# Kernel tuning notes

Hardware: AMD Instinct MI355X
Metric: run time of the kernel (lower is better)

Reference implementation:

```python
import jax, jax.numpy as jnp
import numpy as np

N_USERS = 100000
N_ITEMS = 40000
N_NODES = N_USERS + N_ITEMS
D = 64
IMG_DIM = 2048
TXT_DIM = 384
N_EDGES = 1000000
N_LAYERS = 2
ALPHA = 0.2


def setup_inputs() -> dict:
    key = jax.random.key(0)
    ks = jax.random.split(key, 10)
    edge_index = jax.random.randint(ks[0], (2, N_EDGES), 0, N_NODES, dtype=jnp.int64 if jax.config.jax_enable_x64 else jnp.int32)
    edge_weight = jax.random.uniform(ks[1], (N_EDGES, 1), dtype=jnp.float32)
    image_feats = jax.random.normal(ks[2], (N_ITEMS, IMG_DIM), dtype=jnp.float32)
    text_feats = jax.random.normal(ks[3], (N_ITEMS, TXT_DIM), dtype=jnp.float32)
    s_img = 1.0 / np.sqrt(IMG_DIM)
    s_txt = 1.0 / np.sqrt(TXT_DIM)
    image_trs_w = jax.random.uniform(ks[4], (IMG_DIM, D), jnp.float32, -s_img, s_img)
    image_trs_b = jnp.zeros((D,), jnp.float32)
    text_trs_w = jax.random.uniform(ks[5], (TXT_DIM, D), jnp.float32, -s_txt, s_txt)
    text_trs_b = jnp.zeros((D,), jnp.float32)
    image_pref = jax.random.normal(ks[6], (N_USERS, D), jnp.float32) * 0.1
    text_pref = jax.random.normal(ks[7], (N_USERS, D), jnp.float32) * 0.1
    return {
        "edge_index": edge_index,
        "edge_weight": edge_weight,
        "image_feats": image_feats,
        "text_feats": text_feats,
        "image_trs_w": image_trs_w,
        "image_trs_b": image_trs_b,
        "text_trs_w": text_trs_w,
        "text_trs_b": text_trs_b,
        "image_pref": image_pref,
        "text_pref": text_pref,
    }


def _l2_normalize(x):
    # matches F.normalize(x, p=2, dim=1, eps=1e-12)
    n = jnp.linalg.norm(x, axis=1, keepdims=True)
    return x / jnp.maximum(n, 1e-12)


def _propagate(x, src, dst, w):
    # PyG 'add' aggregation: message = x[src] * w, scatter-add into dst
    msgs = x[src] * w  # [E, D]
    return jax.ops.segment_sum(msgs, dst, num_segments=N_NODES)


def reference(edge_index, edge_weight, image_feats, text_feats,
              image_trs_w, image_trs_b, text_trs_w, text_trs_b,
              image_pref, text_pref):
    src, dst = edge_index[0], edge_index[1]

    image_emb = _l2_normalize(image_feats @ image_trs_w + image_trs_b)
    text_emb = _l2_normalize(text_feats @ text_trs_w + text_trs_b)

    ego_img = jnp.concatenate([image_pref, image_emb], axis=0)  # [N, D]
    ego_txt = jnp.concatenate([text_pref, text_emb], axis=0)    # [N, D]

    for _ in range(N_LAYERS):
        ego_img = _propagate(ego_img, src, dst, edge_weight) + ALPHA * ego_img
        ego_txt = _propagate(ego_txt, src, dst, edge_weight) + ALPHA * ego_txt

    # stack final modality embeddings; rows 0:N_USERS are user preferences,
    # N_USERS: are item embeddings (torch.split boundary)
    return jnp.stack([ego_img, ego_txt], axis=0)  # [2, N, D]
```

## Files before the change

kernel.cpp:

```cpp
#include <hip/hip_runtime.h>

#define N_USERS 100000
#define N_ITEMS 40000
#define NN      140000
#define N_EDGES 1000000
#define ALPHA   0.2f

typedef short bf16x8 __attribute__((ext_vector_type(8)));
typedef float f32x4  __attribute__((ext_vector_type(4)));

__device__ __forceinline__ unsigned short f2b(float x) {
    unsigned u = __builtin_bit_cast(unsigned, x);
    unsigned r = (u + 0x7FFFu + ((u >> 16) & 1u)) >> 16;
    return (unsigned short)r;
}
__device__ __forceinline__ unsigned cvtpk(float lo, float hi) {
    unsigned r;
    asm("v_cvt_pk_bf16_f32 %0, %1, %2" : "=v"(r) : "v"(lo), "v"(hi));
    return r;
}
__device__ __forceinline__ float blo(unsigned u) { return __builtin_bit_cast(float, u << 16); }
__device__ __forceinline__ float bhi(unsigned u) { return __builtin_bit_cast(float, u & 0xFFFF0000u); }

#define PREP_CP   6250
#define PREP_CI   (PREP_CP + 512)
#define PREP_CT   (PREP_CI + 96)
#define PREP_ALL  (PREP_CT + 3907)

__global__ __launch_bounds__(256)
void prep(const float* __restrict__ imgp, const float* __restrict__ txtp,
          unsigned short* __restrict__ X,
          const float* __restrict__ Wi, short* __restrict__ WtImg,
          const float* __restrict__ Wx, short* __restrict__ WtTxt,
          const int* __restrict__ ei, int* __restrict__ deg)
{
    int b = blockIdx.x, t = threadIdx.x;
    if (b < PREP_CP) {
        int tid = b * 256 + t;
        if (tid >= N_USERS * 16) return;
        int i  = tid >> 4;
        int c8 = tid & 15;
        const float* src = (c8 < 8) ? &imgp[(size_t)i * 64 + c8 * 8]
                                    : &txtp[(size_t)i * 64 + (c8 - 8) * 8];
        float4 a = *reinterpret_cast<const float4*>(src);
        float4 c = *reinterpret_cast<const float4*>(src + 4);
        int4 o = make_int4((int)cvtpk(a.x, a.y), (int)cvtpk(a.z, a.w),
                           (int)cvtpk(c.x, c.y), (int)cvtpk(c.z, c.w));
        *reinterpret_cast<int4*>(&X[(size_t)i * 128 + c8 * 8]) = o;
    } else if (b < PREP_CI) {
        int tid = (b - PREP_CP) * 256 + t;
        int k = tid >> 6, n = tid & 63;
        WtImg[(k >> 5) * 2048 + n * 32 + ((k >> 3) & 3) * 8 + (k & 7)] = (short)f2b(Wi[tid]);
    } else if (b < PREP_CT) {
        int tid = (b - PREP_CI) * 256 + t;
        if (tid >= 384 * 64) return;
        int k = tid >> 6, n = tid & 63;
        WtTxt[(k >> 5) * 2048 + n * 32 + ((k >> 3) & 3) * 8 + (k & 7)] = (short)f2b(Wx[tid]);
    } else {
        int e = (b - PREP_CT) * 256 + t;
        if (e < N_EDGES) atomicAdd(&deg[ei[N_EDGES + e]], 1);
    }
}

template<int K, int COLOFF>
__device__ __forceinline__
void gemm_body(int bx, const float* __restrict__ A, const short* __restrict__ Wt,
               const float* __restrict__ bias, unsigned short* __restrict__ X)
{
    constexpr int STEPS = K / 32;
    const int t    = threadIdx.x;
    const int wid  = t >> 6;
    const int lane = t & 63;
    const int lo   = lane & 15;
    const int g    = lane >> 4;
    const int r0w  = bx * 64 + wid * 16;

    const float* Ap  = A + (size_t)(r0w + lo) * K + g * 8;
    const short* Bp0 = Wt + lo * 32 + g * 8;

    f32x4 acc[4];
    #pragma unroll
    for (int ct = 0; ct < 4; ++ct) acc[ct] = (f32x4){0.f, 0.f, 0.f, 0.f};

    float4 xA, yA, xB, yB;
    bf16x8 bA[4], bB[4];

    auto loadA = [&](int s, float4& x, float4& y) {
        const float* p = Ap + s * 32;
        x = *reinterpret_cast<const float4*>(p);
        y = *reinterpret_cast<const float4*>(p + 4);
    };
    auto loadB = [&](int s, bf16x8* bb) {
        const short* p = Bp0 + s * 2048;
        #pragma unroll
        for (int ct = 0; ct < 4; ++ct) {
            int4 w = *reinterpret_cast<const int4*>(p + ct * 512);
            bb[ct] = __builtin_bit_cast(bf16x8, w);
        }
    };
    auto domfma = [&](const float4& x, const float4& y, const bf16x8* bb) {
        int4 ai = make_int4((int)cvtpk(x.x, x.y), (int)cvtpk(x.z, x.w),
                            (int)cvtpk(y.x, y.y), (int)cvtpk(y.z, y.w));
        bf16x8 a = __builtin_bit_cast(bf16x8, ai);
        #pragma unroll
        for (int ct = 0; ct < 4; ++ct)
            acc[ct] = __builtin_amdgcn_mfma_f32_16x16x32_bf16(a, bb[ct], acc[ct], 0, 0, 0);
    };

    loadA(0, xA, yA);
    loadB(0, bA);
    for (int s = 0; s < STEPS; s += 2) {
        loadA(s + 1, xB, yB);
        loadB(s + 1, bB);
        domfma(xA, yA, bA);
        if (s + 2 < STEPS) {
            loadA(s + 2, xA, yA);
            loadB(s + 2, bA);
        }
        domfma(xB, yB, bB);
    }

    float bia[4];
    #pragma unroll
    for (int ct = 0; ct < 4; ++ct) bia[ct] = bias[ct * 16 + lo];

    #pragma unroll
    for (int r = 0; r < 4; ++r) {
        float v[4];
        float ss = 0.f;
        #pragma unroll
        for (int ct = 0; ct < 4; ++ct) { v[ct] = acc[ct][r] + bia[ct]; ss += v[ct] * v[ct]; }
        ss += __shfl_xor(ss, 1);
        ss += __shfl_xor(ss, 2);
        ss += __shfl_xor(ss, 4);
        ss += __shfl_xor(ss, 8);
        float sc = 1.0f / fmaxf(sqrtf(ss), 1e-12f);
        int grow = r0w + g * 4 + r;
        unsigned short* dst = &X[(size_t)(N_USERS + grow) * 128 + COLOFF + lo];
        #pragma unroll
        for (int ct = 0; ct < 4; ++ct) dst[ct * 16] = f2b(v[ct] * sc);
    }
}

__global__ __launch_bounds__(256, 2)
void gemm_fill(const float* __restrict__ Ai, const short* __restrict__ WtImg,
               const float* __restrict__ bi,
               const float* __restrict__ Ax, const short* __restrict__ WtTxt,
               const float* __restrict__ bx, unsigned short* __restrict__ X,
               const int* __restrict__ ei, const float* __restrict__ ew,
               int* __restrict__ cursor, int2* __restrict__ epk)
{
    int b = blockIdx.x;
    if (b < 625)       gemm_body<2048, 0 >(b, Ai, WtImg, bi, X);
    else if (b < 1250) gemm_body< 384, 64>(b - 625, Ax, WtTxt, bx, X);
    else {
        int e = (b - 1250) * 256 + threadIdx.x;
        if (e >= N_EDGES) return;
        int s = ei[e];
        int d = ei[N_EDGES + e];
        int p = atomicAdd(&cursor[d], 1);
        epk[p] = make_int2(s, __builtin_bit_cast(int, ew[e]));
    }
}

__global__ void scan1(const int* __restrict__ deg, int* __restrict__ row_ptr,
                      int* __restrict__ blockSums)
{
    __shared__ int ts[256];
    int t = threadIdx.x, b = blockIdx.x;
    int base = b * 1024 + t * 4;
    int v[4]; int s = 0;
    #pragma unroll
    for (int j = 0; j < 4; j++) {
        v[j] = (base + j < NN) ? deg[base + j] : 0;
        s += v[j];
    }
    ts[t] = s;
    __syncthreads();
    for (int off = 1; off < 256; off <<= 1) {
        int x = (t >= off) ? ts[t - off] : 0;
        __syncthreads();
        ts[t] += x;
        __syncthreads();
    }
    int excl = ts[t] - s;
    int run = excl;
    #pragma unroll
    for (int j = 0; j < 4; j++) {
        if (base + j < NN) row_ptr[base + j] = run;
        run += v[j];
    }
    if (t == 255) blockSums[b] = ts[255];
}

__global__ void scan23(const int* __restrict__ blockSums, int* __restrict__ row_ptr,
                       int* __restrict__ cursor)
{
    __shared__ int ts[256];
    int t = threadIdx.x, b = blockIdx.x;
    ts[t] = (t < b) ? blockSums[t] : 0;
    __syncthreads();
    for (int off = 128; off > 0; off >>= 1) {
        if (t < off) ts[t] += ts[t + off];
        __syncthreads();
    }
    int off0 = ts[0];
    int base = b * 1024 + t * 4;
    #pragma unroll
    for (int j = 0; j < 4; j++) {
        int idx = base + j;
        if (idx < NN) {
            int r = row_ptr[idx] + off0;
            row_ptr[idx] = r;
            cursor[idx]  = r;
        }
    }
    if (b == 0 && t == 0) row_ptr[NN] = N_EDGES;
}

template<bool FINAL>
__global__ __launch_bounds__(256)
void propagate(const unsigned short* __restrict__ Xin, const int* __restrict__ row_ptr,
               const int2* __restrict__ epk, void* __restrict__ outv)
{
    int wid  = threadIdx.x >> 6;
    int lane = threadIdx.x & 63;
    int node = blockIdx.x * 4 + wid;
    if (node >= NN) return;
    int e0 = row_ptr[node];
    int e1 = row_ptr[node + 1];
    float accx = 0.f, accy = 0.f;
    for (int base = e0; base < e1; base += 64) {
        int cnt = e1 - base; if (cnt > 64) cnt = 64;
        int sv = 0, wvb = 0;
        if (base + lane < e1) {
            int2 ev = epk[base + lane];
            sv = ev.x; wvb = ev.y;
        }
        float wv = __builtin_bit_cast(float, wvb);
        int i = 0;
        for (; i + 3 < cnt; i += 4) {
            int   s0 = __shfl(sv, i),     s1 = __shfl(sv, i + 1);
            int   s2 = __shfl(sv, i + 2), s3 = __shfl(sv, i + 3);
            float w0 = __shfl(wv, i),     w1 = __shfl(wv, i + 1);
            float w2 = __shfl(wv, i + 2), w3 = __shfl(wv, i + 3);
            unsigned u0 = *reinterpret_cast<const unsigned*>(&Xin[(size_t)s0 * 128 + lane * 2]);
            unsigned u1 = *reinterpret_cast<const unsigned*>(&Xin[(size_t)s1 * 128 + lane * 2]);
            unsigned u2 = *reinterpret_cast<const unsigned*>(&Xin[(size_t)s2 * 128 + lane * 2]);
            unsigned u3 = *reinterpret_cast<const unsigned*>(&Xin[(size_t)s3 * 128 + lane * 2]);
            accx = fmaf(w0, blo(u0), accx); accy = fmaf(w0, bhi(u0), accy);
            accx = fmaf(w1, blo(u1), accx); accy = fmaf(w1, bhi(u1), accy);
            accx = fmaf(w2, blo(u2), accx); accy = fmaf(w2, bhi(u2), accy);
            accx = fmaf(w3, blo(u3), accx); accy = fmaf(w3, bhi(u3), accy);
        }
        for (; i < cnt; ++i) {
            int   s0 = __shfl(sv, i);
            float w0 = __shfl(wv, i);
            unsigned u0 = *reinterpret_cast<const unsigned*>(&Xin[(size_t)s0 * 128 + lane * 2]);
            accx = fmaf(w0, blo(u0), accx); accy = fmaf(w0, bhi(u0), accy);
        }
    }
    unsigned us = *reinterpret_cast<const unsigned*>(&Xin[(size_t)node * 128 + lane * 2]);
    accx += ALPHA * blo(us);
    accy += ALPHA * bhi(us);
    if (!FINAL) {
        unsigned short* out = (unsigned short*)outv;
        *reinterpret_cast<unsigned*>(&out[(size_t)node * 128 + lane * 2]) = cvtpk(accx, accy);
    } else {
        float* out = (float*)outv;
        int d = lane * 2;
        float* dst = (d < 64) ? &out[(size_t)node * 64 + d]
                              : &out[(size_t)NN * 64 + (size_t)node * 64 + (d - 64)];
        *reinterpret_cast<float2*>(dst) = make_float2(accx, accy);
    }
}

extern "C" void kernel_launch(void* const* d_in, const int* in_sizes, int n_in,
                              void* d_out, int out_size, void* d_ws, size_t ws_size,
                              hipStream_t stream)
{
    const int*   ei       = (const int*)d_in[0];
    const float* ew       = (const float*)d_in[1];
    const float* img_feat = (const float*)d_in[2];
    const float* txt_feat = (const float*)d_in[3];
    const float* img_w    = (const float*)d_in[4];
    const float* img_b    = (const float*)d_in[5];
    const float* txt_w    = (const float*)d_in[6];
    const float* txt_b    = (const float*)d_in[7];
    const float* img_pref = (const float*)d_in[8];
    const float* txt_pref = (const float*)d_in[9];
    float* out = (float*)d_out;

    const size_t XBYTES = (size_t)NN * 128 * 2;
    char* ws = (char*)d_ws;
    size_t off = 0;
    auto alloc = [&](size_t bytes) -> void* {
        void* p = ws + off;
        off = (off + bytes + 255) & ~(size_t)255;
        return p;
    };
    unsigned short* Xa = (unsigned short*)alloc(XBYTES);
    unsigned short* Xb = (unsigned short*)alloc(XBYTES);
    int*   deg     = (int*)alloc((size_t)NN * 4);
    int*   row_ptr = (int*)alloc((size_t)(NN + 1) * 4);
    int*   cursor  = (int*)alloc((size_t)NN * 4);
    int2*  epk     = (int2*)alloc((size_t)N_EDGES * 8);
    int*   bsums   = (int*)alloc(256 * 4);
    short* WtImg   = (short*)alloc((size_t)2048 * 64 * 2);
    short* WtTxt   = (short*)alloc((size_t)384 * 64 * 2);

    hipMemsetAsync(deg, 0, (size_t)NN * 4, stream);

    prep<<<PREP_ALL, 256, 0, stream>>>(img_pref, txt_pref, Xa,
                                       img_w, WtImg, txt_w, WtTxt, ei, deg);

    scan1<<<137, 256, 0, stream>>>(deg, row_ptr, bsums);
    scan23<<<137, 256, 0, stream>>>(bsums, row_ptr, cursor);

    gemm_fill<<<1250 + 3907, 256, 0, stream>>>(img_feat, WtImg, img_b,
                                               txt_feat, WtTxt, txt_b, Xa,
                                               ei, ew, cursor, epk);

    propagate<false><<<35000, 256, 0, stream>>>(Xa, row_ptr, epk, Xb);
    propagate<true ><<<35000, 256, 0, stream>>>(Xb, row_ptr, epk, out);
}
```

Before: 342.5 us.

## Stage GEMM A tiles through LDS with direct global-to-LDS loads and swizzle

The feature-projection GEMM now copies 64x64 fp32 tiles of the input matrix into shared memory with global_load_lds, double-buffered and XOR-swizzled, instead of each lane reading strided rows straight from global memory into registers. The aim is coalesced, asynchronous loads of the 328 MB image/text feature reads and fewer bank conflicts. The cost is 32 KB of LDS per block, a block barrier on every k-tile, and a dropped min-blocks launch bound, all of which can lower occupancy. The edge-fill blocks in the same kernel also reserve that LDS even though they never use it.

```diff
diff --git a/kernel.cpp b/kernel.cpp
--- a/kernel.cpp
+++ b/kernel.cpp
@@ -21,6 +21,12 @@
 }
 __device__ __forceinline__ float blo(unsigned u) { return __builtin_bit_cast(float, u << 16); }
 __device__ __forceinline__ float bhi(unsigned u) { return __builtin_bit_cast(float, u & 0xFFFF0000u); }
+
+__device__ __forceinline__ void gl_lds16(const float* g, float* l) {
+    __builtin_amdgcn_global_load_lds(
+        (const __attribute__((address_space(1))) void*)g,
+        (__attribute__((address_space(3))) void*)l, 16, 0, 0);
+}
 
 #define PREP_CP   6250
 #define PREP_CI   (PREP_CP + 512)
@@ -65,65 +71,70 @@
 template<int K, int COLOFF>
 __device__ __forceinline__
 void gemm_body(int bx, const float* __restrict__ A, const short* __restrict__ Wt,
-               const float* __restrict__ bias, unsigned short* __restrict__ X)
-{
-    constexpr int STEPS = K / 32;
+               const float* __restrict__ bias, unsigned short* __restrict__ X,
+               float* lds)
+{
+    constexpr int NT = K / 64;
     const int t    = threadIdx.x;
     const int wid  = t >> 6;
     const int lane = t & 63;
     const int lo   = lane & 15;
     const int g    = lane >> 4;
-    const int r0w  = bx * 64 + wid * 16;
-
-    const float* Ap  = A + (size_t)(r0w + lo) * K + g * 8;
+    const int r0   = bx * 64;
+
     const short* Bp0 = Wt + lo * 32 + g * 8;
 
     f32x4 acc[4];
     #pragma unroll
     for (int ct = 0; ct < 4; ++ct) acc[ct] = (f32x4){0.f, 0.f, 0.f, 0.f};
 
-    float4 xA, yA, xB, yB;
-    bf16x8 bA[4], bB[4];
-
-    auto loadA = [&](int s, float4& x, float4& y) {
-        const float* p = Ap + s * 32;
-        x = *reinterpret_cast<const float4*>(p);
-        y = *reinterpret_cast<const float4*>(p + 4);
+    auto stage = [&](int buf, int kt) {
+        int k0 = kt * 64;
+        #pragma unroll
+        for (int i = 0; i < 4; ++i) {
+            int c     = i * 4 + wid;
+            int row_t = c * 4 + g;
+            int u_log = lo ^ (row_t & 15);
+            const float* gp = A + (size_t)(r0 + row_t) * K + k0 + u_log * 4;
+            gl_lds16(gp, lds + buf * 4096 + c * 256);
+        }
     };
-    auto loadB = [&](int s, bf16x8* bb) {
-        const short* p = Bp0 + s * 2048;
+
+    auto compute = [&](int buf, int kt) {
+        int row_t = wid * 16 + lo;
+        const float* base = lds + buf * 4096 + row_t * 64;
         #pragma unroll
-        for (int ct = 0; ct < 4; ++ct) {
-            int4 w = *reinterpret_cast<const int4*>(p + ct * 512);
-            bb[ct] = __builtin_bit_cast(bf16x8, w);
+        for (int m = 0; m < 2; ++m) {
+            int u0 = (m * 8 + 2 * g) ^ lo;
+            int u1 = (m * 8 + 2 * g + 1) ^ lo;
+            float4 xa = *reinterpret_cast<const float4*>(base + u0 * 4);
+            float4 ya = *reinterpret_cast<const float4*>(base + u1 * 4);
+            int4 ai = make_int4((int)cvtpk(xa.x, xa.y), (int)cvtpk(xa.z, xa.w),
+                                (int)cvtpk(ya.x, ya.y), (int)cvtpk(ya.z, ya.w));
+            bf16x8 a = __builtin_bit_cast(bf16x8, ai);
+            const short* p = Bp0 + (size_t)(kt * 2 + m) * 2048;
+            #pragma unroll
+            for (int ct = 0; ct < 4; ++ct) {
+                int4 w = *reinterpret_cast<const int4*>(p + ct * 512);
+                bf16x8 bb = __builtin_bit_cast(bf16x8, w);
+                acc[ct] = __builtin_amdgcn_mfma_f32_16x16x32_bf16(a, bb, acc[ct], 0, 0, 0);
+            }
         }
     };
-    auto domfma = [&](const float4& x, const float4& y, const bf16x8* bb) {
-        int4 ai = make_int4((int)cvtpk(x.x, x.y), (int)cvtpk(x.z, x.w),
-                            (int)cvtpk(y.x, y.y), (int)cvtpk(y.z, y.w));
-        bf16x8 a = __builtin_bit_cast(bf16x8, ai);
-        #pragma unroll
-        for (int ct = 0; ct < 4; ++ct)
-            acc[ct] = __builtin_amdgcn_mfma_f32_16x16x32_bf16(a, bb[ct], acc[ct], 0, 0, 0);
-    };
-
-    loadA(0, xA, yA);
-    loadB(0, bA);
-    for (int s = 0; s < STEPS; s += 2) {
-        loadA(s + 1, xB, yB);
-        loadB(s + 1, bB);
-        domfma(xA, yA, bA);
-        if (s + 2 < STEPS) {
-            loadA(s + 2, xA, yA);
-            loadB(s + 2, bA);
-        }
-        domfma(xB, yB, bB);
+
+    stage(0, 0);
+    __syncthreads();
+    for (int kt = 0; kt < NT; ++kt) {
+        if (kt + 1 < NT) stage((kt + 1) & 1, kt + 1);
+        compute(kt & 1, kt);
+        __syncthreads();
     }
 
     float bia[4];
     #pragma unroll
     for (int ct = 0; ct < 4; ++ct) bia[ct] = bias[ct * 16 + lo];
 
+    int r0w = r0 + wid * 16;
     #pragma unroll
     for (int r = 0; r < 4; ++r) {
         float v[4];
@@ -142,7 +153,7 @@
     }
 }
 
-__global__ __launch_bounds__(256, 2)
+__global__ __launch_bounds__(256)
 void gemm_fill(const float* __restrict__ Ai, const short* __restrict__ WtImg,
                const float* __restrict__ bi,
                const float* __restrict__ Ax, const short* __restrict__ WtTxt,
@@ -150,9 +161,10 @@
                const int* __restrict__ ei, const float* __restrict__ ew,
                int* __restrict__ cursor, int2* __restrict__ epk)
 {
+    __shared__ float lds[8192];
     int b = blockIdx.x;
-    if (b < 625)       gemm_body<2048, 0 >(b, Ai, WtImg, bi, X);
-    else if (b < 1250) gemm_body< 384, 64>(b - 625, Ax, WtTxt, bx, X);
+    if (b < 625)       gemm_body<2048, 0 >(b, Ai, WtImg, bi, X, lds);
+    else if (b < 1250) gemm_body< 384, 64>(b - 625, Ax, WtTxt, bx, X, lds);
     else {
         int e = (b - 1250) * 256 + threadIdx.x;
         if (e >= N_EDGES) return;
```

After: 326.6 us. 1.05x faster.
